# Performance work log

Hardware: AMD Instinct MI355X
Metric: run time of the kernel (lower is better)

The kernel has to match this reference:

```python
import jax, jax.numpy as jnp
import numpy as np

HIDDEN = 512
HEADS = 8
HEAD_DIM = HIDDEN // HEADS


def setup_inputs() -> dict:
    key = jax.random.key(0)
    ks = jax.random.split(key, 9)
    B, S = 4, 2048
    scale = 1.0 / np.sqrt(HIDDEN)
    x = jax.random.normal(ks[0], (B, S, HIDDEN), dtype=jnp.float32)
    Wq = jax.random.normal(ks[1], (HIDDEN, HIDDEN), dtype=jnp.float32) * scale
    Wk = jax.random.normal(ks[2], (HIDDEN, HIDDEN), dtype=jnp.float32) * scale
    Wv = jax.random.normal(ks[3], (HIDDEN, HIDDEN), dtype=jnp.float32) * scale
    Wo = jax.random.normal(ks[4], (HIDDEN, HIDDEN), dtype=jnp.float32) * scale
    bq = jax.random.normal(ks[5], (HIDDEN,), dtype=jnp.float32) * 0.01
    bk = jax.random.normal(ks[6], (HIDDEN,), dtype=jnp.float32) * 0.01
    bv = jax.random.normal(ks[7], (HIDDEN,), dtype=jnp.float32) * 0.01
    bo = jax.random.normal(ks[8], (HIDDEN,), dtype=jnp.float32) * 0.01
    return {"x": x, "Wq": Wq, "bq": bq, "Wk": Wk, "bk": bk,
            "Wv": Wv, "bv": bv, "Wo": Wo, "bo": bo}


def reference(x, Wq, bq, Wk, bk, Wv, bv, Wo, bo):
    B, S, _ = x.shape
    # project and split heads: [B, H, S, D]
    def split_heads(t):
        return t.reshape(B, S, HEADS, HEAD_DIM).transpose(0, 2, 1, 3)
    Q = split_heads(x @ Wq.T + bq)
    K = split_heads(x @ Wk.T + bk)
    V = split_heads(x @ Wv.T + bv)
    scores = jnp.einsum("bhsd,bhtd->bhst", Q, K) / jnp.sqrt(
        jnp.array(HEAD_DIM, dtype=x.dtype))
    attn = jax.nn.softmax(scores, axis=-1)  # dropout is identity in eval
    ctx = jnp.einsum("bhst,bhtd->bhsd", attn, V)
    ctx = ctx.transpose(0, 2, 1, 3).reshape(B, S, HIDDEN)
    return ctx @ Wo.T + bo
```

## Files before the change

kernel.cpp:

```cpp
#include <hip/hip_runtime.h>
#include <stdint.h>

#define HID 512
#define NH 8
#define HD 64
#define BB 4
#define SS 2048

typedef unsigned short u16;
typedef __attribute__((ext_vector_type(8))) short short8;
typedef __attribute__((ext_vector_type(4))) float f32x4;

#define MFMA16(a, b, c) __builtin_amdgcn_mfma_f32_16x16x32_bf16((a), (b), (c), 0, 0, 0)

__device__ __forceinline__ u16 f2bf(float f) {
  union { float f; uint32_t u; } v; v.f = f;
  return (u16)((v.u + 0x7fffu + ((v.u >> 16) & 1u)) >> 16);
}

__device__ __forceinline__ void gl_lds16(const u16* g, u16* l) {
  __builtin_amdgcn_global_load_lds(
      (const __attribute__((address_space(1))) unsigned int*)g,
      (__attribute__((address_space(3))) unsigned int*)l, 16, 0, 0);
}

__global__ void prep(const float* __restrict__ x,
                     const float* __restrict__ w0, const float* __restrict__ w1,
                     const float* __restrict__ w2, const float* __restrict__ w3,
                     u16* __restrict__ xb,
                     u16* __restrict__ o0, u16* __restrict__ o1,
                     u16* __restrict__ o2, u16* __restrict__ o3) {
  const int bid = blockIdx.x;
  const float* in;
  u16* out;
  int base;
  if (bid < 4096) {
    in = x; out = xb; base = bid * 1024;
  } else {
    const int z = (bid - 4096) >> 8;
    base = ((bid - 4096) & 255) * 1024;
    in = (z == 0) ? w0 : (z == 1) ? w1 : (z == 2) ? w2 : w3;
    out = (z == 0) ? o0 : (z == 1) ? o1 : (z == 2) ? o2 : o3;
  }
  const int i = base + threadIdx.x * 4;
  float4 v = *(const float4*)(in + i);
  ushort4 o;
  o.x = f2bf(v.x); o.y = f2bf(v.y); o.z = f2bf(v.z); o.w = f2bf(v.w);
  *(ushort4*)(out + i) = o;
}

__global__ __launch_bounds__(256, 3)
void qkv_gemm(const u16* __restrict__ xb,
              const u16* __restrict__ wq, const u16* __restrict__ wk, const u16* __restrict__ wv,
              const float* __restrict__ bq, const float* __restrict__ bk, const float* __restrict__ bv,
              u16* __restrict__ Q, u16* __restrict__ K, u16* __restrict__ Vt) {
  __shared__ u16 sA[128 * 32];
  __shared__ u16 sB[128 * 32];
  __shared__ u16 sT[128 * 136];
  const int tid = threadIdx.x;
  const int lane = tid & 63;
  const int wave = tid >> 6;
  const int l15 = lane & 15;
  const int quad = lane >> 4;
  const int wm = wave >> 1, wn = wave & 1;
  const int bm = blockIdx.x, bn = blockIdx.y, z = blockIdx.z;

  const u16* W = (z == 0) ? wq : (z == 1) ? wk : wv;
  const float* bias = (z == 0) ? bq : (z == 1) ? bk : bv;
  const float scale = (z == 0) ? 0.18033688011112042f : 1.0f;

  const int srow = tid >> 2;
  const int sg = (tid & 3) ^ ((srow >> 1) & 3);
  const u16* gA = xb + (bm * 128 + srow) * 512 + sg * 8;
  const u16* gB = W + (bn * 128 + srow) * 512 + sg * 8;

  const int fsw = (quad ^ ((l15 >> 1) & 3)) * 8;
  int aoff[4], boff[4];
#pragma unroll
  for (int t = 0; t < 4; ++t) {
    aoff[t] = (wm * 64 + t * 16 + l15) * 32 + fsw;
    boff[t] = (wn * 64 + t * 16 + l15) * 32 + fsw;
  }

  f32x4 acc[4][4] = {};

  for (int kk = 0; kk < 16; ++kk) {
    const int k0 = kk * 32;
    gl_lds16(gA + k0, &sA[wave * 512]);
    gl_lds16(gA + k0 + 64 * 512, &sA[2048 + wave * 512]);
    gl_lds16(gB + k0, &sB[wave * 512]);
    gl_lds16(gB + k0 + 64 * 512, &sB[2048 + wave * 512]);
    __syncthreads();
    short8 af[4], bf[4];
#pragma unroll
    for (int t = 0; t < 4; ++t) af[t] = *(const short8*)&sA[aoff[t]];
#pragma unroll
    for (int t = 0; t < 4; ++t) bf[t] = *(const short8*)&sB[boff[t]];
#pragma unroll
    for (int mi = 0; mi < 4; ++mi)
#pragma unroll
      for (int ni = 0; ni < 4; ++ni)
        acc[mi][ni] = MFMA16(af[mi], bf[ni], acc[mi][ni]);
    __syncthreads();
  }

  if (z != 2) {
    u16* dst = (z == 0) ? Q : K;
#pragma unroll
    for (int mi = 0; mi < 4; ++mi) {
#pragma unroll
      for (int ni = 0; ni < 4; ++ni) {
        const int col = bn * 128 + wn * 64 + ni * 16 + l15;
        const float bs = bias[col];
#pragma unroll
        for (int i = 0; i < 4; ++i) {
          const int row = bm * 128 + wm * 64 + mi * 16 + quad * 4 + i;
          const float v = (acc[mi][ni][i] + bs) * scale;
          const int b = row >> 11, s = row & 2047;
          const int h = col >> 6, d = col & 63;
          dst[(((size_t)(b * 8 + h) * 2048 + s) << 6) + d] = f2bf(v);
        }
      }
    }
  } else {
#pragma unroll
    for (int mi = 0; mi < 4; ++mi) {
#pragma unroll
      for (int ni = 0; ni < 4; ++ni) {
        const int cl = wn * 64 + ni * 16 + l15;
        const float bs = bias[bn * 128 + cl];
#pragma unroll
        for (int i = 0; i < 4; ++i) {
          const int rl = wm * 64 + mi * 16 + quad * 4 + i;
          sT[cl * 136 + rl] = f2bf(acc[mi][ni][i] + bs);
        }
      }
    }
    __syncthreads();
    const int cl = tid >> 1;
    const int half = tid & 1;
    const int b = bm >> 4;
    const int h = bn * 2 + (cl >> 6);
    const int d = cl & 63;
    const int s0 = (bm & 15) * 128 + half * 64;
    u16* dst = Vt + (((size_t)(b * 8 + h) * 64 + d) << 11) + s0;
    const u16* src = &sT[cl * 136 + half * 64];
#pragma unroll
    for (int k = 0; k < 8; ++k)
      *(short8*)(dst + k * 8) = *(const short8*)(src + k * 8);
  }
}

__global__ __launch_bounds__(256, 2)
void attn(const u16* __restrict__ Q, const u16* __restrict__ K,
          const u16* __restrict__ Vt, u16* __restrict__ ctx) {
  __shared__ u16 sK[2][8192];
  __shared__ u16 sV[2][8192];
  __shared__ u16 sP[8192];
  const int tid = threadIdx.x;
  const int lane = tid & 63;
  const int wave = tid >> 6;
  const int l15 = lane & 15;
  const int quad = lane >> 4;
  const int qt = blockIdx.x;
  const int bh = blockIdx.y;

  const u16* Qb = Q + (size_t)bh * SS * HD;
  const u16* Kb = K + (size_t)bh * SS * HD;
  const u16* Vb = Vt + (size_t)bh * HD * SS;

  short8 qf[2][2];
#pragma unroll
  for (int mi = 0; mi < 2; ++mi)
#pragma unroll
    for (int kc = 0; kc < 2; ++kc) {
      const int r = qt * 128 + wave * 32 + mi * 16 + l15;
      qf[mi][kc] = *(const short8*)(Qb + r * 64 + kc * 32 + quad * 8);
    }

  short8 ones;
#pragma unroll
  for (int j = 0; j < 8; ++j) ones[j] = (short)0x3F80;

  f32x4 oacc[2][4] = {};
  f32x4 lsum[2] = {};

  int xp[2];
#pragma unroll
  for (int kt = 0; kt < 2; ++kt) xp[kt] = ((kt * 4 + quad) ^ (l15 & 7)) * 8;
  const int prow0 = (wave * 32 + l15) * 64;
  const int prow1 = prow0 + 16 * 64;

  const int tK = tid >> 3;
  const int dcK = (tid & 7) ^ (tK & 7);
  const u16* gK = Kb + tK * 64 + dcK * 8;
  const int dV = tid >> 4;
  const int tgV = (tid & 15) ^ dV;
  const u16* gV = Vb + dV * 2048 + tgV * 8;

#pragma unroll
  for (int it = 0; it < 4; ++it) {
    gl_lds16(gK + it * 2048, &sK[0][it * 2048 + wave * 512]);
    gl_lds16(gV + it * 32768, &sV[0][it * 2048 + wave * 512]);
  }
  __syncthreads();

  for (int tt = 0; tt < 16; ++tt) {
    const int cur = tt & 1;
    if (tt < 15) {
      const int nxt = cur ^ 1;
#pragma unroll
      for (int it = 0; it < 4; ++it) {
        gl_lds16(gK + (tt + 1) * 8192 + it * 2048, &sK[nxt][it * 2048 + wave * 512]);
        gl_lds16(gV + (tt + 1) * 128 + it * 32768, &sV[nxt][it * 2048 + wave * 512]);
      }
    }

#pragma unroll
    for (int h = 0; h < 2; ++h) {
      f32x4 sacc[2][4] = {};
#pragma unroll
      for (int ni = 0; ni < 4; ++ni) {
        const int nig = h * 4 + ni;
        const short8 b0 = *(const short8*)&sK[cur][(nig * 16 + l15) * 64 + ((quad) ^ (l15 & 7)) * 8];
        const short8 b1 = *(const short8*)&sK[cur][(nig * 16 + l15) * 64 + ((4 + quad) ^ (l15 & 7)) * 8];
        sacc[0][ni] = MFMA16(qf[0][0], b0, sacc[0][ni]);
        sacc[0][ni] = MFMA16(qf[0][1], b1, sacc[0][ni]);
        sacc[1][ni] = MFMA16(qf[1][0], b0, sacc[1][ni]);
        sacc[1][ni] = MFMA16(qf[1][1], b1, sacc[1][ni]);
      }

#pragma unroll
      for (int mi = 0; mi < 2; ++mi) {
#pragma unroll
        for (int i = 0; i < 4; ++i) {
          const int wrow = wave * 32 + mi * 16 + quad * 4 + i;
          const int rx7 = (quad * 4 + i) & 7;
          const int base = wrow * 64 + (l15 & 7);
#pragma unroll
          for (int ni = 0; ni < 4; ++ni) {
            const float p = __builtin_amdgcn_exp2f(sacc[mi][ni][i]);
            const uint32_t u = __builtin_bit_cast(uint32_t, p);
            sP[base + (((ni * 2 + (l15 >> 3)) ^ rx7) << 3)] = (u16)(u >> 16);
          }
        }
      }

#pragma unroll
      for (int kt = 0; kt < 2; ++kt) {
        const short8 a0 = *(const short8*)&sP[prow0 + xp[kt]];
        const short8 a1 = *(const short8*)&sP[prow1 + xp[kt]];
        lsum[0] = MFMA16(a0, ones, lsum[0]);
        lsum[1] = MFMA16(a1, ones, lsum[1]);
#pragma unroll
        for (int nd = 0; nd < 4; ++nd) {
          const short8 bvv = *(const short8*)&sV[cur][(nd * 16 + l15) * 128 +
                                                     ((h * 8 + kt * 4 + quad) ^ l15) * 8];
          oacc[0][nd] = MFMA16(a0, bvv, oacc[0][nd]);
          oacc[1][nd] = MFMA16(a1, bvv, oacc[1][nd]);
        }
      }
    }
    __syncthreads();
  }

  float inv[2][4];
#pragma unroll
  for (int mi = 0; mi < 2; ++mi)
#pragma unroll
    for (int i = 0; i < 4; ++i) inv[mi][i] = __builtin_amdgcn_rcpf(lsum[mi][i]);

  const int b = bh >> 3, h = bh & 7;
#pragma unroll
  for (int mi = 0; mi < 2; ++mi)
#pragma unroll
    for (int nd = 0; nd < 4; ++nd)
#pragma unroll
      for (int i = 0; i < 4; ++i) {
        const int s = qt * 128 + wave * 32 + mi * 16 + quad * 4 + i;
        const int d = nd * 16 + l15;
        const float v = oacc[mi][nd][i] * inv[mi][i];
        ctx[((size_t)(b * 2048 + s) << 9) + h * 64 + d] = f2bf(v);
      }
}

__global__ __launch_bounds__(256, 2)
void out_gemm(const u16* __restrict__ A, const u16* __restrict__ W,
              const float* __restrict__ bias, float* __restrict__ out) {
  __shared__ u16 sA[128 * 32];
  __shared__ u16 sB[64 * 32];
  const int tid = threadIdx.x;
  const int lane = tid & 63;
  const int wave = tid >> 6;
  const int l15 = lane & 15;
  const int quad = lane >> 4;
  const int bm = blockIdx.x, bn = blockIdx.y;

  const int srow = tid >> 2;
  const int sg = (tid & 3) ^ ((srow >> 1) & 3);
  const u16* gA = A + (bm * 128 + srow) * 512 + sg * 8;
  const u16* gB = W + (bn * 64 + srow) * 512 + sg * 8;

  const int fsw = (quad ^ ((l15 >> 1) & 3)) * 8;
  int aoff[2], boff[4];
#pragma unroll
  for (int t = 0; t < 2; ++t) aoff[t] = (wave * 32 + t * 16 + l15) * 32 + fsw;
#pragma unroll
  for (int t = 0; t < 4; ++t) boff[t] = (t * 16 + l15) * 32 + fsw;

  f32x4 acc[2][4] = {};

  for (int kk = 0; kk < 16; ++kk) {
    const int k0 = kk * 32;
    gl_lds16(gA + k0, &sA[wave * 512]);
    gl_lds16(gA + k0 + 64 * 512, &sA[2048 + wave * 512]);
    gl_lds16(gB + k0, &sB[wave * 512]);
    __syncthreads();
    short8 af[2], bf[4];
#pragma unroll
    for (int t = 0; t < 2; ++t) af[t] = *(const short8*)&sA[aoff[t]];
#pragma unroll
    for (int t = 0; t < 4; ++t) bf[t] = *(const short8*)&sB[boff[t]];
#pragma unroll
    for (int mi = 0; mi < 2; ++mi)
#pragma unroll
      for (int ni = 0; ni < 4; ++ni)
        acc[mi][ni] = MFMA16(af[mi], bf[ni], acc[mi][ni]);
    __syncthreads();
  }

#pragma unroll
  for (int mi = 0; mi < 2; ++mi) {
#pragma unroll
    for (int ni = 0; ni < 4; ++ni) {
      const int col = bn * 64 + ni * 16 + l15;
      const float bs = bias[col];
#pragma unroll
      for (int i = 0; i < 4; ++i) {
        const int row = bm * 128 + wave * 32 + mi * 16 + quad * 4 + i;
        out[(size_t)row * 512 + col] = acc[mi][ni][i] + bs;
      }
    }
  }
}

extern "C" void kernel_launch(void* const* d_in, const int* in_sizes, int n_in,
                              void* d_out, int out_size, void* d_ws, size_t ws_size,
                              hipStream_t stream) {
  const float* x = (const float*)d_in[0];
  const float* Wq = (const float*)d_in[1];
  const float* bq = (const float*)d_in[2];
  const float* Wk = (const float*)d_in[3];
  const float* bk = (const float*)d_in[4];
  const float* Wv = (const float*)d_in[5];
  const float* bv = (const float*)d_in[6];
  const float* Wo = (const float*)d_in[7];
  const float* bo = (const float*)d_in[8];
  float* out = (float*)d_out;

  char* ws = (char*)d_ws;
  u16* xb  = (u16*)(ws);
  u16* wqb = (u16*)(ws + (8u << 20));
  u16* wkb = (u16*)(ws + (8u << 20) + (512u << 10));
  u16* wvb = (u16*)(ws + (9u << 20));
  u16* wob = (u16*)(ws + (9u << 20) + (512u << 10));
  u16* Qb  = (u16*)(ws + (10u << 20));
  u16* Kb  = (u16*)(ws + (18u << 20));
  u16* Vtb = (u16*)(ws + (26u << 20));
  u16* ctx = (u16*)(ws + (34u << 20));

  prep<<<5120, 256, 0, stream>>>(x, Wq, Wk, Wv, Wo, xb, wqb, wkb, wvb, wob);
  qkv_gemm<<<dim3(64, 4, 3), 256, 0, stream>>>(xb, wqb, wkb, wvb, bq, bk, bv, Qb, Kb, Vtb);
  attn<<<dim3(16, 32), 256, 0, stream>>>(Qb, Kb, Vtb, ctx);
  out_gemm<<<dim3(64, 8), 256, 0, stream>>>(ctx, wob, bo, out);
}
```

Baseline: 166.9 us.

## Double-buffer GEMM loads, compute V transposed directly, restructure attention to 8 waves

The QKV and output GEMMs now double-buffer their LDS tiles, so the next K-slice loads while the current one is multiplied. The V projection swaps operands (Wv rows as A, x as B) so each tile lands already transposed and is written straight to Vt, dropping the LDS transpose buffer. Attention moves to 512-thread blocks with 8 waves of 16 query rows each and 64-key tiles over 32 iterations, cutting LDS and register use per block. The direct Vt stores are narrow scattered 2-byte writes, and the attention loop now hits its barrier twice as often.

```diff
diff --git a/kernel.cpp b/kernel.cpp
--- a/kernel.cpp
+++ b/kernel.cpp
@@ -54,25 +54,28 @@
               const u16* __restrict__ wq, const u16* __restrict__ wk, const u16* __restrict__ wv,
               const float* __restrict__ bq, const float* __restrict__ bk, const float* __restrict__ bv,
               u16* __restrict__ Q, u16* __restrict__ K, u16* __restrict__ Vt) {
-  __shared__ u16 sA[128 * 32];
-  __shared__ u16 sB[128 * 32];
-  __shared__ u16 sT[128 * 136];
+  __shared__ u16 sA[2][128 * 32];
+  __shared__ u16 sB[2][128 * 32];
   const int tid = threadIdx.x;
   const int lane = tid & 63;
   const int wave = tid >> 6;
   const int l15 = lane & 15;
   const int quad = lane >> 4;
   const int wm = wave >> 1, wn = wave & 1;
-  const int bm = blockIdx.x, bn = blockIdx.y, z = blockIdx.z;
-
-  const u16* W = (z == 0) ? wq : (z == 1) ? wk : wv;
+  const int z = blockIdx.z;
+
   const float* bias = (z == 0) ? bq : (z == 1) ? bk : bv;
   const float scale = (z == 0) ? 0.18033688011112042f : 1.0f;
 
+  const u16* Arows = (z == 2) ? wv : xb;
+  const u16* Brows = (z == 2) ? xb : ((z == 0) ? wq : wk);
+  const int am0 = (z == 2) ? (blockIdx.y * 128) : (blockIdx.x * 128);
+  const int bn0 = (z == 2) ? (blockIdx.x * 128) : (blockIdx.y * 128);
+
   const int srow = tid >> 2;
   const int sg = (tid & 3) ^ ((srow >> 1) & 3);
-  const u16* gA = xb + (bm * 128 + srow) * 512 + sg * 8;
-  const u16* gB = W + (bn * 128 + srow) * 512 + sg * 8;
+  const u16* gA = Arows + (am0 + srow) * 512 + sg * 8;
+  const u16* gB = Brows + (bn0 + srow) * 512 + sg * 8;
 
   const int fsw = (quad ^ ((l15 >> 1) & 3)) * 8;
   int aoff[4], boff[4];
@@ -84,18 +87,27 @@
 
   f32x4 acc[4][4] = {};
 
+  gl_lds16(gA, &sA[0][wave * 512]);
+  gl_lds16(gA + 64 * 512, &sA[0][2048 + wave * 512]);
+  gl_lds16(gB, &sB[0][wave * 512]);
+  gl_lds16(gB + 64 * 512, &sB[0][2048 + wave * 512]);
+  __syncthreads();
+
   for (int kk = 0; kk < 16; ++kk) {
-    const int k0 = kk * 32;
-    gl_lds16(gA + k0, &sA[wave * 512]);
-    gl_lds16(gA + k0 + 64 * 512, &sA[2048 + wave * 512]);
-    gl_lds16(gB + k0, &sB[wave * 512]);
-    gl_lds16(gB + k0 + 64 * 512, &sB[2048 + wave * 512]);
-    __syncthreads();
+    const int cur = kk & 1;
+    if (kk < 15) {
+      const int nxt = cur ^ 1;
+      const int k0 = (kk + 1) * 32;
+      gl_lds16(gA + k0, &sA[nxt][wave * 512]);
+      gl_lds16(gA + k0 + 64 * 512, &sA[nxt][2048 + wave * 512]);
+      gl_lds16(gB + k0, &sB[nxt][wave * 512]);
+      gl_lds16(gB + k0 + 64 * 512, &sB[nxt][2048 + wave * 512]);
+    }
     short8 af[4], bf[4];
 #pragma unroll
-    for (int t = 0; t < 4; ++t) af[t] = *(const short8*)&sA[aoff[t]];
-#pragma unroll
-    for (int t = 0; t < 4; ++t) bf[t] = *(const short8*)&sB[boff[t]];
+    for (int t = 0; t < 4; ++t) af[t] = *(const short8*)&sA[cur][aoff[t]];
+#pragma unroll
+    for (int t = 0; t < 4; ++t) bf[t] = *(const short8*)&sB[cur][boff[t]];
 #pragma unroll
     for (int mi = 0; mi < 4; ++mi)
 #pragma unroll
@@ -110,11 +122,11 @@
     for (int mi = 0; mi < 4; ++mi) {
 #pragma unroll
       for (int ni = 0; ni < 4; ++ni) {
-        const int col = bn * 128 + wn * 64 + ni * 16 + l15;
+        const int col = bn0 + wn * 64 + ni * 16 + l15;
         const float bs = bias[col];
 #pragma unroll
         for (int i = 0; i < 4; ++i) {
-          const int row = bm * 128 + wm * 64 + mi * 16 + quad * 4 + i;
+          const int row = am0 + wm * 64 + mi * 16 + quad * 4 + i;
           const float v = (acc[mi][ni][i] + bs) * scale;
           const int b = row >> 11, s = row & 2047;
           const int h = col >> 6, d = col & 63;
@@ -126,37 +138,27 @@
 #pragma unroll
     for (int mi = 0; mi < 4; ++mi) {
 #pragma unroll
-      for (int ni = 0; ni < 4; ++ni) {
-        const int cl = wn * 64 + ni * 16 + l15;
-        const float bs = bias[bn * 128 + cl];
-#pragma unroll
-        for (int i = 0; i < 4; ++i) {
-          const int rl = wm * 64 + mi * 16 + quad * 4 + i;
-          sT[cl * 136 + rl] = f2bf(acc[mi][ni][i] + bs);
+      for (int i = 0; i < 4; ++i) {
+        const int o = am0 + wm * 64 + mi * 16 + quad * 4 + i;
+        const float bs = bias[o];
+        const int h = o >> 6, d = o & 63;
+#pragma unroll
+        for (int ni = 0; ni < 4; ++ni) {
+          const int r = bn0 + wn * 64 + ni * 16 + l15;
+          const int b = r >> 11, s = r & 2047;
+          Vt[(((size_t)(b * 8 + h) * 64 + d) << 11) + s] = f2bf(acc[mi][ni][i] + bs);
         }
       }
     }
-    __syncthreads();
-    const int cl = tid >> 1;
-    const int half = tid & 1;
-    const int b = bm >> 4;
-    const int h = bn * 2 + (cl >> 6);
-    const int d = cl & 63;
-    const int s0 = (bm & 15) * 128 + half * 64;
-    u16* dst = Vt + (((size_t)(b * 8 + h) * 64 + d) << 11) + s0;
-    const u16* src = &sT[cl * 136 + half * 64];
-#pragma unroll
-    for (int k = 0; k < 8; ++k)
-      *(short8*)(dst + k * 8) = *(const short8*)(src + k * 8);
-  }
-}
-
-__global__ __launch_bounds__(256, 2)
+  }
+}
+
+__global__ __launch_bounds__(512, 4)
 void attn(const u16* __restrict__ Q, const u16* __restrict__ K,
           const u16* __restrict__ Vt, u16* __restrict__ ctx) {
-  __shared__ u16 sK[2][8192];
-  __shared__ u16 sV[2][8192];
-  __shared__ u16 sP[8192];
+  __shared__ u16 sK[2][64 * 64];
+  __shared__ u16 sV[2][64 * 64];
+  __shared__ u16 sP[128 * 64];
   const int tid = threadIdx.x;
   const int lane = tid & 63;
   const int wave = tid >> 6;
@@ -169,126 +171,99 @@
   const u16* Kb = K + (size_t)bh * SS * HD;
   const u16* Vb = Vt + (size_t)bh * HD * SS;
 
-  short8 qf[2][2];
-#pragma unroll
-  for (int mi = 0; mi < 2; ++mi)
-#pragma unroll
-    for (int kc = 0; kc < 2; ++kc) {
-      const int r = qt * 128 + wave * 32 + mi * 16 + l15;
-      qf[mi][kc] = *(const short8*)(Qb + r * 64 + kc * 32 + quad * 8);
-    }
+  short8 qf[2];
+  {
+    const int r = qt * 128 + wave * 16 + l15;
+    qf[0] = *(const short8*)(Qb + r * 64 + quad * 8);
+    qf[1] = *(const short8*)(Qb + r * 64 + 32 + quad * 8);
+  }
 
   short8 ones;
 #pragma unroll
   for (int j = 0; j < 8; ++j) ones[j] = (short)0x3F80;
 
-  f32x4 oacc[2][4] = {};
-  f32x4 lsum[2] = {};
-
+  f32x4 oacc[4] = {};
+  f32x4 lsum = {};
+
+  const int prow = (wave * 16 + l15) * 64;
   int xp[2];
 #pragma unroll
   for (int kt = 0; kt < 2; ++kt) xp[kt] = ((kt * 4 + quad) ^ (l15 & 7)) * 8;
-  const int prow0 = (wave * 32 + l15) * 64;
-  const int prow1 = prow0 + 16 * 64;
 
   const int tK = tid >> 3;
   const int dcK = (tid & 7) ^ (tK & 7);
   const u16* gK = Kb + tK * 64 + dcK * 8;
-  const int dV = tid >> 4;
-  const int tgV = (tid & 15) ^ dV;
-  const u16* gV = Vb + dV * 2048 + tgV * 8;
-
-#pragma unroll
-  for (int it = 0; it < 4; ++it) {
-    gl_lds16(gK + it * 2048, &sK[0][it * 2048 + wave * 512]);
-    gl_lds16(gV + it * 32768, &sV[0][it * 2048 + wave * 512]);
-  }
+  const u16* gV = Vb + tK * 2048 + dcK * 8;
+
+  gl_lds16(gK, &sK[0][wave * 512]);
+  gl_lds16(gV, &sV[0][wave * 512]);
   __syncthreads();
 
-  for (int tt = 0; tt < 16; ++tt) {
+  for (int tt = 0; tt < 32; ++tt) {
     const int cur = tt & 1;
-    if (tt < 15) {
+    if (tt < 31) {
       const int nxt = cur ^ 1;
-#pragma unroll
-      for (int it = 0; it < 4; ++it) {
-        gl_lds16(gK + (tt + 1) * 8192 + it * 2048, &sK[nxt][it * 2048 + wave * 512]);
-        gl_lds16(gV + (tt + 1) * 128 + it * 32768, &sV[nxt][it * 2048 + wave * 512]);
-      }
-    }
-
-#pragma unroll
-    for (int h = 0; h < 2; ++h) {
-      f32x4 sacc[2][4] = {};
+      gl_lds16(gK + (tt + 1) * 4096, &sK[nxt][wave * 512]);
+      gl_lds16(gV + (tt + 1) * 64, &sV[nxt][wave * 512]);
+    }
+
+    f32x4 sacc[4] = {};
+#pragma unroll
+    for (int ni = 0; ni < 4; ++ni) {
+      const short8 b0 = *(const short8*)&sK[cur][(ni * 16 + l15) * 64 + ((quad) ^ (l15 & 7)) * 8];
+      const short8 b1 = *(const short8*)&sK[cur][(ni * 16 + l15) * 64 + ((4 + quad) ^ (l15 & 7)) * 8];
+      sacc[ni] = MFMA16(qf[0], b0, sacc[ni]);
+      sacc[ni] = MFMA16(qf[1], b1, sacc[ni]);
+    }
+
+#pragma unroll
+    for (int i = 0; i < 4; ++i) {
+      const int wrow = wave * 16 + quad * 4 + i;
+      const int rx7 = (quad * 4 + i) & 7;
+      const int base = wrow * 64 + (l15 & 7);
 #pragma unroll
       for (int ni = 0; ni < 4; ++ni) {
-        const int nig = h * 4 + ni;
-        const short8 b0 = *(const short8*)&sK[cur][(nig * 16 + l15) * 64 + ((quad) ^ (l15 & 7)) * 8];
-        const short8 b1 = *(const short8*)&sK[cur][(nig * 16 + l15) * 64 + ((4 + quad) ^ (l15 & 7)) * 8];
-        sacc[0][ni] = MFMA16(qf[0][0], b0, sacc[0][ni]);
-        sacc[0][ni] = MFMA16(qf[0][1], b1, sacc[0][ni]);
-        sacc[1][ni] = MFMA16(qf[1][0], b0, sacc[1][ni]);
-        sacc[1][ni] = MFMA16(qf[1][1], b1, sacc[1][ni]);
-      }
-
-#pragma unroll
-      for (int mi = 0; mi < 2; ++mi) {
-#pragma unroll
-        for (int i = 0; i < 4; ++i) {
-          const int wrow = wave * 32 + mi * 16 + quad * 4 + i;
-          const int rx7 = (quad * 4 + i) & 7;
-          const int base = wrow * 64 + (l15 & 7);
-#pragma unroll
-          for (int ni = 0; ni < 4; ++ni) {
-            const float p = __builtin_amdgcn_exp2f(sacc[mi][ni][i]);
-            const uint32_t u = __builtin_bit_cast(uint32_t, p);
-            sP[base + (((ni * 2 + (l15 >> 3)) ^ rx7) << 3)] = (u16)(u >> 16);
-          }
-        }
-      }
-
-#pragma unroll
-      for (int kt = 0; kt < 2; ++kt) {
-        const short8 a0 = *(const short8*)&sP[prow0 + xp[kt]];
-        const short8 a1 = *(const short8*)&sP[prow1 + xp[kt]];
-        lsum[0] = MFMA16(a0, ones, lsum[0]);
-        lsum[1] = MFMA16(a1, ones, lsum[1]);
-#pragma unroll
-        for (int nd = 0; nd < 4; ++nd) {
-          const short8 bvv = *(const short8*)&sV[cur][(nd * 16 + l15) * 128 +
-                                                     ((h * 8 + kt * 4 + quad) ^ l15) * 8];
-          oacc[0][nd] = MFMA16(a0, bvv, oacc[0][nd]);
-          oacc[1][nd] = MFMA16(a1, bvv, oacc[1][nd]);
-        }
+        const float p = __builtin_amdgcn_exp2f(sacc[ni][i]);
+        const uint32_t u = __builtin_bit_cast(uint32_t, p);
+        sP[base + (((ni * 2 + (l15 >> 3)) ^ rx7) << 3)] = (u16)(u >> 16);
+      }
+    }
+
+#pragma unroll
+    for (int kt = 0; kt < 2; ++kt) {
+      const short8 a = *(const short8*)&sP[prow + xp[kt]];
+      lsum = MFMA16(a, ones, lsum);
+#pragma unroll
+      for (int nd = 0; nd < 4; ++nd) {
+        const short8 bvv = *(const short8*)&sV[cur][(nd * 16 + l15) * 64 +
+                                                   ((kt * 4 + quad) ^ (l15 & 7)) * 8];
+        oacc[nd] = MFMA16(a, bvv, oacc[nd]);
       }
     }
     __syncthreads();
   }
 
-  float inv[2][4];
-#pragma unroll
-  for (int mi = 0; mi < 2; ++mi)
-#pragma unroll
-    for (int i = 0; i < 4; ++i) inv[mi][i] = __builtin_amdgcn_rcpf(lsum[mi][i]);
+  float inv[4];
+#pragma unroll
+  for (int i = 0; i < 4; ++i) inv[i] = __builtin_amdgcn_rcpf(lsum[i]);
 
   const int b = bh >> 3, h = bh & 7;
 #pragma unroll
-  for (int mi = 0; mi < 2; ++mi)
-#pragma unroll
-    for (int nd = 0; nd < 4; ++nd)
-#pragma unroll
-      for (int i = 0; i < 4; ++i) {
-        const int s = qt * 128 + wave * 32 + mi * 16 + quad * 4 + i;
-        const int d = nd * 16 + l15;
-        const float v = oacc[mi][nd][i] * inv[mi][i];
-        ctx[((size_t)(b * 2048 + s) << 9) + h * 64 + d] = f2bf(v);
-      }
+  for (int nd = 0; nd < 4; ++nd)
+#pragma unroll
+    for (int i = 0; i < 4; ++i) {
+      const int s = qt * 128 + wave * 16 + quad * 4 + i;
+      const int d = nd * 16 + l15;
+      const float v = oacc[nd][i] * inv[i];
+      ctx[((size_t)(b * 2048 + s) << 9) + h * 64 + d] = f2bf(v);
+    }
 }
 
 __global__ __launch_bounds__(256, 2)
 void out_gemm(const u16* __restrict__ A, const u16* __restrict__ W,
               const float* __restrict__ bias, float* __restrict__ out) {
-  __shared__ u16 sA[128 * 32];
-  __shared__ u16 sB[64 * 32];
+  __shared__ u16 sA[2][128 * 32];
+  __shared__ u16 sB[2][64 * 32];
   const int tid = threadIdx.x;
   const int lane = tid & 63;
   const int wave = tid >> 6;
@@ -310,17 +285,25 @@
 
   f32x4 acc[2][4] = {};
 
+  gl_lds16(gA, &sA[0][wave * 512]);
+  gl_lds16(gA + 64 * 512, &sA[0][2048 + wave * 512]);
+  gl_lds16(gB, &sB[0][wave * 512]);
+  __syncthreads();
+
   for (int kk = 0; kk < 16; ++kk) {
-    const int k0 = kk * 32;
-    gl_lds16(gA + k0, &sA[wave * 512]);
-    gl_lds16(gA + k0 + 64 * 512, &sA[2048 + wave * 512]);
-    gl_lds16(gB + k0, &sB[wave * 512]);
-    __syncthreads();
+    const int cur = kk & 1;
+    if (kk < 15) {
+      const int nxt = cur ^ 1;
+      const int k0 = (kk + 1) * 32;
+      gl_lds16(gA + k0, &sA[nxt][wave * 512]);
+      gl_lds16(gA + k0 + 64 * 512, &sA[nxt][2048 + wave * 512]);
+      gl_lds16(gB + k0, &sB[nxt][wave * 512]);
+    }
     short8 af[2], bf[4];
 #pragma unroll
-    for (int t = 0; t < 2; ++t) af[t] = *(const short8*)&sA[aoff[t]];
-#pragma unroll
-    for (int t = 0; t < 4; ++t) bf[t] = *(const short8*)&sB[boff[t]];
+    for (int t = 0; t < 2; ++t) af[t] = *(const short8*)&sA[cur][aoff[t]];
+#pragma unroll
+    for (int t = 0; t < 4; ++t) bf[t] = *(const short8*)&sB[cur][boff[t]];
 #pragma unroll
     for (int mi = 0; mi < 2; ++mi)
 #pragma unroll
@@ -371,6 +354,6 @@
 
   prep<<<5120, 256, 0, stream>>>(x, Wq, Wk, Wv, Wo, xb, wqb, wkb, wvb, wob);
   qkv_gemm<<<dim3(64, 4, 3), 256, 0, stream>>>(xb, wqb, wkb, wvb, bq, bk, bv, Qb, Kb, Vtb);
-  attn<<<dim3(16, 32), 256, 0, stream>>>(Qb, Kb, Vtb, ctx);
+  attn<<<dim3(16, 32), 512, 0, stream>>>(Qb, Kb, Vtb, ctx);
   out_gemm<<<dim3(64, 8), 256, 0, stream>>>(ctx, wob, bo, out);
 }
```

Result: no change. 169.6 us (+1.6%).
